# Kernel optimization log

Measured on AMD Instinct MI355X. Metric: run time of the kernel, lower is better.

## Reference

```python
import jax, jax.numpy as jnp
import numpy as np

B, S, H = 2, 2048, 4096
NH, NKV, HD = 32, 8, 128
ROPE_THETA = 10000.0


def _rope_tables(seq_len, head_dim, theta):
    inv_freq = 1.0 / (theta ** (jnp.arange(0, head_dim, 2, dtype=jnp.float32) / head_dim))
    t = jnp.arange(seq_len, dtype=jnp.float32)
    freqs = jnp.outer(t, inv_freq)            # [S, HD/2]
    emb = jnp.concatenate([freqs, freqs], axis=-1)  # [S, HD]
    return jnp.cos(emb), jnp.sin(emb)


def _rotate_half(x):
    x1, x2 = jnp.split(x, 2, axis=-1)
    return jnp.concatenate([-x2, x1], axis=-1)


def setup_inputs() -> dict:
    key = jax.random.key(0)
    ks = jax.random.split(key, 5)
    hidden_states = jax.random.normal(ks[0], (B, S, H), dtype=jnp.float32)
    # causal additive mask [B,1,S,S]
    neg = jnp.finfo(jnp.float32).min
    causal = jnp.where(jnp.tril(jnp.ones((S, S), dtype=bool)), 0.0, neg)
    attention_mask = jnp.broadcast_to(causal[None, None], (B, 1, S, S)).astype(jnp.float32)
    position_ids = jnp.broadcast_to(jnp.arange(S, dtype=jnp.int64)[None], (B, S))
    scale = 0.02
    Wq = jax.random.normal(ks[1], (H, H), dtype=jnp.float32) * scale
    Wk = jax.random.normal(ks[2], (NKV * HD, H), dtype=jnp.float32) * scale
    Wv = jax.random.normal(ks[3], (NKV * HD, H), dtype=jnp.float32) * scale
    Wo = jax.random.normal(ks[4], (H, H), dtype=jnp.float32) * scale
    return {"hidden_states": hidden_states, "attention_mask": attention_mask,
            "position_ids": position_ids, "Wq": Wq, "Wk": Wk, "Wv": Wv, "Wo": Wo}


def reference(hidden_states, attention_mask, position_ids, Wq, Wk, Wv, Wo):
    bsz, q_len, _ = hidden_states.shape
    # projections (nn.Linear: x @ W.T)
    q = (hidden_states @ Wq.T).reshape(bsz, q_len, NH, HD).transpose(0, 2, 1, 3)    # [B,NH,S,HD]
    k = (hidden_states @ Wk.T).reshape(bsz, q_len, NKV, HD).transpose(0, 2, 1, 3)   # [B,NKV,S,HD]
    v = (hidden_states @ Wv.T).reshape(bsz, q_len, NKV, HD).transpose(0, 2, 1, 3)
    # RoPE
    cos, sin = _rope_tables(q_len, HD, ROPE_THETA)
    cos = cos[position_ids][:, None]   # [B,1,S,HD]
    sin = sin[position_ids][:, None]
    q = q * cos + _rotate_half(q) * sin
    k = k * cos + _rotate_half(k) * sin
    # repeat_kv (GQA): [B,NKV,S,HD] -> [B,NH,S,HD]
    n_rep = NH // NKV
    k = jnp.repeat(k, n_rep, axis=1)
    v = jnp.repeat(v, n_rep, axis=1)
    # attention
    attn = jnp.einsum('bhqd,bhkd->bhqk', q, k) / jnp.sqrt(jnp.float32(HD))
    attn = attn + attention_mask
    attn = jax.nn.softmax(attn.astype(jnp.float32), axis=-1).astype(q.dtype)
    out = jnp.einsum('bhqk,bhkd->bhqd', attn, v)           # [B,NH,S,HD]
    out = out.transpose(0, 2, 1, 3).reshape(bsz, q_len, NH * HD)
    return out @ Wo.T
```

## Files before the change

kernel.cpp:

```cpp
#include <hip/hip_runtime.h>
#include <hip/hip_bf16.h>


typedef __bf16 bf16;
typedef __bf16 bf16x8 __attribute__((ext_vector_type(8)));
typedef float f32x4 __attribute__((ext_vector_type(4)));

#define UNROLL _Pragma("unroll")

__device__ __forceinline__ void async16(const bf16* g, bf16* l) {
  __builtin_amdgcn_global_load_lds(
      (const __attribute__((address_space(1))) void*)g,
      (__attribute__((address_space(3))) void*)l,
      16, 0, 0);
}

#define BARR { __builtin_amdgcn_s_barrier(); }
#define VMCNT(n) { asm volatile("s_waitcnt vmcnt(" #n ")" ::: "memory"); }

__global__ void k_cvt(const float* __restrict__ s, bf16* __restrict__ d, int n8) {
  int i = blockIdx.x * 256 + threadIdx.x;
  if (i >= n8) return;
  const float4* sp = (const float4*)s + (size_t)i * 2;
  float4 a = sp[0], b = sp[1];
  bf16x8 o = { (bf16)a.x, (bf16)a.y, (bf16)a.z, (bf16)a.w,
               (bf16)b.x, (bf16)b.y, (bf16)b.z, (bf16)b.w };
  *(bf16x8*)(d + (size_t)i * 8) = o;
}

__global__ void k_cvtw3(const float* __restrict__ Wq, const float* __restrict__ Wk,
                        const float* __restrict__ Wv, bf16* __restrict__ Wqkv) {
  int u = blockIdx.x * 256 + threadIdx.x;
  const float* sp;
  bf16* dp;
  size_t off;
  if (u < 2097152) { sp = Wq; dp = Wqkv; off = u; }
  else if (u < 2621440) { sp = Wk; dp = Wqkv + 16777216u; off = u - 2097152; }
  else { sp = Wv; dp = Wqkv + 20971520u; off = u - 2621440; }
  const float4* s4 = (const float4*)sp + off * 2;
  float4 a = s4[0], b = s4[1];
  bf16x8 o = { (bf16)a.x, (bf16)a.y, (bf16)a.z, (bf16)a.w,
               (bf16)b.x, (bf16)b.y, (bf16)b.z, (bf16)b.w };
  *(bf16x8*)(dp + off * 8) = o;
}

template <typename OutT, int SPLIT>
__global__ __launch_bounds__(512, 2) void k_gemmCS(
    const bf16* __restrict__ A, const bf16* __restrict__ Bw,
    OutT* __restrict__ C, int lda, int Kloop, int ldc, int nbx, size_t csplit) {
  __shared__ __align__(16) bf16 lds[2][4][8192];
  const int tid = threadIdx.x;
  const int lane = tid & 63;
  const int w = tid >> 6;
  const int wm = w >> 2, wn = w & 3;
  const int l16 = lane & 15, lh = lane >> 4;

  const int cpx = gridDim.x >> 3;
  const int swz = (blockIdx.x & 7) * cpx + (blockIdx.x >> 3);
  int by, bx;
  if (SPLIT) {
    const int kh = swz >> 7;
    const int t = swz & 127;
    by = t >> 3;
    bx = t & 7;
    A += (size_t)kh * 2048;
    Bw += (size_t)kh * 2048;
    C += (size_t)kh * csplit;
  } else {
    by = swz / nbx;
    bx = swz % nbx;
  }
  const size_t m0 = (size_t)by * 256, n0 = (size_t)bx * 256;

  const int row0 = tid >> 2;
  const int cOff = ((tid & 3) ^ ((row0 >> 1) & 3)) * 8;
  const bf16* pA0 = A + (m0 + row0) * lda + cOff;
  const bf16* pA1 = pA0 + (size_t)128 * lda;
  const bf16* pB0 = Bw + (n0 + row0) * lda + cOff;
  const bf16* pB1 = pB0 + (size_t)128 * lda;

#define SA(s, h, t)                                        \
  { const int kk = (t) * 64 + (h) * 32;                    \
    async16(pA0 + kk, &lds[s][h][0] + tid * 8);            \
    async16(pA1 + kk, &lds[s][h][0] + 4096 + tid * 8); }
#define SB(s, h, t)                                        \
  { const int kk = (t) * 64 + (h) * 32;                    \
    async16(pB0 + kk, &lds[s][2 + (h)][0] + tid * 8);      \
    async16(pB1 + kk, &lds[s][2 + (h)][0] + 4096 + tid * 8); }

#define RDA(s, u, mh)                                                 \
  UNROLL for (int x = 0; x < 4; ++x) {                                \
    int p = (wm * 128 + (mh) * 64 + x * 16 + l16) * 64 + lh * 16;     \
    p ^= ((p >> 7) & 3) << 4;                                         \
    Ar[x] = *(const bf16x8*)((const char*)&lds[s][u][0] + p);         \
  }
#define RDB(s, u)                                                     \
  UNROLL for (int y = 0; y < 4; ++y) {                                \
    int p = (wn * 64 + y * 16 + l16) * 64 + lh * 16;                  \
    p ^= ((p >> 7) & 3) << 4;                                         \
    Br[y] = *(const bf16x8*)((const char*)&lds[s][u][0] + p);         \
  }
#define MF(mh)                                                        \
  { __builtin_amdgcn_s_setprio(1);                                    \
    UNROLL for (int x = 0; x < 4; ++x)                                \
      UNROLL for (int y = 0; y < 4; ++y)                              \
        acc[(mh) * 4 + x][y] = __builtin_amdgcn_mfma_f32_16x16x32_bf16( \
            Ar[x], Br[y], acc[(mh) * 4 + x][y], 0, 0, 0);             \
    __builtin_amdgcn_s_setprio(0); }

  f32x4 acc[8][4] = {};
  const int NITER = Kloop >> 7;

  SA(0, 0, 0); SB(0, 0, 0); SA(0, 1, 0); SB(0, 1, 0); SA(1, 0, 1); SB(1, 0, 1);
  VMCNT(8);

#define ITER_BODY(i, LAST)                                                  \
  { const int t0 = 2 * (i), t1 = t0 + 1;                                    \
    bf16x8 Ar[4], Br[4];                                                    \
    BARR; RDA(0, 0, 0); RDB(0, 2); SA(1, 1, t1); MF(0);                     \
    BARR; RDA(0, 0, 1); SB(1, 1, t1); MF(1); VMCNT(8);                      \
    BARR; RDA(0, 1, 0); RDB(0, 3); if (!(LAST)) SA(0, 0, t0 + 2); MF(0);    \
    BARR; RDA(0, 1, 1); if (!(LAST)) SB(0, 0, t0 + 2); MF(1);               \
    if (LAST) { VMCNT(4); } else { VMCNT(8); }                              \
    BARR; RDA(1, 0, 0); RDB(1, 2); if (!(LAST)) SA(0, 1, t0 + 2); MF(0);    \
    BARR; RDA(1, 0, 1); if (!(LAST)) SB(0, 1, t0 + 2); MF(1);               \
    if (LAST) { VMCNT(0); } else { VMCNT(8); }                              \
    BARR; RDA(1, 1, 0); RDB(1, 3); if (!(LAST)) SA(1, 0, t1 + 2); MF(0);    \
    BARR; RDA(1, 1, 1); if (!(LAST)) SB(1, 0, t1 + 2); MF(1);               \
    if (!(LAST)) VMCNT(8); }

  for (int i = 0; i < NITER - 1; ++i) ITER_BODY(i, 0);
  ITER_BODY(NITER - 1, 1);

  UNROLL for (int mi = 0; mi < 8; ++mi) {
    size_t row = m0 + wm * 128 + mi * 16 + lh * 4;
    UNROLL for (int ni = 0; ni < 4; ++ni) {
      size_t col = n0 + wn * 64 + ni * 16 + l16;
      UNROLL for (int j = 0; j < 4; ++j)
        C[(row + j) * ldc + col] = (OutT)acc[mi][ni][j];
    }
  }
#undef SA
#undef SB
#undef RDA
#undef RDB
#undef MF
#undef ITER_BODY
}

__global__ void k_redsum(const bf16* __restrict__ s, bf16* __restrict__ QKV) {
  int i = blockIdx.x * 256 + threadIdx.x;
  int e = i * 8;
  int tok = e >> 11;
  int c = e & 2047;
  bf16x8 a = *(const bf16x8*)(s + e);
  bf16x8 b = *(const bf16x8*)(s + 8388608 + e);
  bf16x8 o;
  UNROLL for (int j = 0; j < 8; ++j) o[j] = (bf16)((float)a[j] + (float)b[j]);
  *(bf16x8*)(QKV + (size_t)tok * 6144 + 4096 + c) = o;
}

__global__ void k_rope(const bf16* __restrict__ QKV, bf16* __restrict__ Qr,
                       bf16* __restrict__ Kr) {
  int gid = blockIdx.x * 256 + threadIdx.x;
  int seg = gid & 7;
  int rest = gid >> 3;
  int slot = rest % 40;
  int tok = rest / 40;
  int s = tok & 2047;
  int b = tok >> 11;
  const bf16* src = QKV + (size_t)tok * 6144 + slot * 128 + seg * 8;
  bf16x8 a = *(const bf16x8*)src;
  bf16x8 c = *(const bf16x8*)(src + 64);
  bf16x8 o1v, o2v;
  const float scale = (slot < 32) ? 0.08838834764831845f : 1.0f;
  UNROLL for (int j = 0; j < 8; ++j) {
    int p = seg * 8 + j;
    float f = exp2f((float)p * (-13.287712379549449f / 64.0f));
    float sn, cn;
    sincosf((float)s * f, &sn, &cn);
    float x1 = (float)a[j], x2 = (float)c[j];
    o1v[j] = (bf16)((x1 * cn - x2 * sn) * scale);
    o2v[j] = (bf16)((x2 * cn + x1 * sn) * scale);
  }
  bf16* dst;
  if (slot < 32) {
    dst = Qr + (((size_t)b * 32 + slot) * 2048 + s) * 128 + seg * 8;
  } else {
    dst = Kr + (((size_t)b * 8 + (slot - 32)) * 2048 + s) * 128 + seg * 8;
  }
  *(bf16x8*)dst = o1v;
  *(bf16x8*)(dst + 64) = o2v;
}

__global__ void k_vtrans(const bf16* __restrict__ QKV, bf16* __restrict__ Vtg) {
  __shared__ __align__(16) bf16 T[64 * 64];
  const int tid = threadIdx.x;
  const int dt = blockIdx.x & 1;
  const int st = (blockIdx.x >> 1) & 31;
  const int hh = blockIdx.x >> 6;
  const int hkv = hh & 7, b = hh >> 3;
  const int s0 = st * 64, d0 = dt * 64;
  const bf16* src = QKV + (size_t)(b * 2048 + s0) * 6144 + 5120 + hkv * 128 + d0;
  UNROLL for (int k = 0; k < 2; ++k) {
    int cc = tid * 2 + k;
    int r = cc >> 3, c8 = cc & 7;
    bf16x8 v = *(const bf16x8*)(src + (size_t)r * 6144 + c8 * 8);
    int byte = (r * 128 + c8 * 16) ^ ((r & 7) << 4);
    *(bf16x8*)((char*)T + byte) = v;
  }
  __syncthreads();
  bf16* dst = Vtg + ((size_t)(b * 8 + hkv) * 128 + d0) * 2048 + s0;
  UNROLL for (int k = 0; k < 2; ++k) {
    int cc = tid * 2 + k;
    int d = cc >> 3, s8 = cc & 7;
    bf16x8 v;
    UNROLL for (int j = 0; j < 8; ++j) {
      int s = s8 * 8 + j;
      int byte = (s * 128 + d * 2) ^ ((s & 7) << 4);
      v[j] = *(const bf16*)((const char*)T + byte);
    }
    *(bf16x8*)(dst + (size_t)d * 2048 + s8 * 8) = v;
  }
}

__global__ __launch_bounds__(256, 2) void k_flash(
    const bf16* __restrict__ Qr, const bf16* __restrict__ Kr,
    const bf16* __restrict__ Vtg, bf16* __restrict__ Out) {
  __shared__ __align__(16) bf16 Kl[2][64 * 128];
  __shared__ __align__(16) bf16 Vl[2][128 * 64];
  __shared__ __align__(16) bf16 Pl[4][32 * 64];
  const int tid = threadIdx.x;
  const int lane = tid & 63;
  const int w = tid >> 6;
  const int l16 = lane & 15, lh = lane >> 4;
  const int bid = blockIdx.x;
  const int stream = ((bid >> 8) << 3) | (bid & 7);
  const int inner = (bid >> 3) & 31;
  const int b = stream >> 3;
  const int hkv = stream & 7;
  const int h = hkv * 4 + (inner >> 3);
  const int pid = inner & 7;
  const bf16* Kbase = Kr + ((size_t)stream) * 2048 * 128;
  const bf16* Vbase = Vtg + ((size_t)stream) * 128 * 2048;
  bf16* P = &Pl[w][0];

  int kOff[4], vOff[4], ldsOff[4];
  UNROLL for (int i = 0; i < 4; ++i) {
    int c = (w * 4 + i) * 64 + lane;
    ldsOff[i] = c * 8;
    int r = c >> 4, p = c & 15;
    kOff[i] = r * 128 + (p ^ (r & 7)) * 8;
    int r2 = c >> 3, p2 = c & 7;
    vOff[i] = r2 * 2048 + (p2 ^ (r2 & 7)) * 8;
  }

  for (int qi = 0; qi < 2; ++qi) {
    const int q = qi ? (15 - pid) : pid;
    const int q0 = q * 128;
    const int nt = 2 * q + 2;

    bf16x8 qf[2][4];
    UNROLL for (int m = 0; m < 2; ++m) {
      const bf16* qb = Qr + (((size_t)(b * 32 + h)) * 2048 + q0 + w * 32 + m * 16 + l16) * 128 + lh * 8;
      UNROLL for (int kc = 0; kc < 4; ++kc) qf[m][kc] = *(const bf16x8*)(qb + kc * 32);
    }
    f32x4 acc[2][8] = {};
    float mrow[2][4] = {{-1e30f, -1e30f, -1e30f, -1e30f}, {-1e30f, -1e30f, -1e30f, -1e30f}};
    float lrow[2][4] = {};

    UNROLL for (int i = 0; i < 4; ++i) {
      async16(Kbase + kOff[i], &Kl[0][0] + ldsOff[i]);
      async16(Vbase + vOff[i], &Vl[0][0] + ldsOff[i]);
    }
    __syncthreads();

    for (int t = 0; t < nt; ++t) {
      const int cur = t & 1;
      if (t + 1 < nt) {
        const int nb = t + 1;
        UNROLL for (int i = 0; i < 4; ++i) {
          async16(Kbase + (size_t)nb * 8192 + kOff[i], &Kl[cur ^ 1][0] + ldsOff[i]);
          async16(Vbase + (size_t)nb * 64 + vOff[i], &Vl[cur ^ 1][0] + ldsOff[i]);
        }
      }
      f32x4 sf[2][4] = {};
      UNROLL for (int ni = 0; ni < 4; ++ni) {
        int row = ni * 16 + l16;
        bf16x8 kf[4];
        UNROLL for (int kc = 0; kc < 4; ++kc) {
          int byte = (row * 256 + kc * 64 + lh * 16) ^ ((row & 7) << 4);
          kf[kc] = *(const bf16x8*)((const char*)&Kl[cur][0] + byte);
        }
        UNROLL for (int m = 0; m < 2; ++m)
          UNROLL for (int kc = 0; kc < 4; ++kc)
            sf[m][ni] = __builtin_amdgcn_mfma_f32_16x16x32_bf16(qf[m][kc], kf[kc], sf[m][ni], 0, 0, 0);
      }
      if (t >= 2 * q) {
        UNROLL for (int m = 0; m < 2; ++m)
          UNROLL for (int ni = 0; ni < 4; ++ni) {
            int key = t * 64 + ni * 16 + l16;
            UNROLL for (int j = 0; j < 4; ++j) {
              int rowg = q0 + w * 32 + m * 16 + lh * 4 + j;
              if (key > rowg) sf[m][ni][j] = -1e30f;
            }
          }
      }
      float corr[2][4];
      UNROLL for (int m = 0; m < 2; ++m)
        UNROLL for (int j = 0; j < 4; ++j) {
          float mx = fmaxf(fmaxf(sf[m][0][j], sf[m][1][j]), fmaxf(sf[m][2][j], sf[m][3][j]));
          mx = fmaxf(mx, __shfl_xor(mx, 1));
          mx = fmaxf(mx, __shfl_xor(mx, 2));
          mx = fmaxf(mx, __shfl_xor(mx, 4));
          mx = fmaxf(mx, __shfl_xor(mx, 8));
          float mn = fmaxf(mrow[m][j], mx);
          corr[m][j] = __expf(mrow[m][j] - mn);
          mrow[m][j] = mn;
          float rs = 0.f;
          UNROLL for (int ni = 0; ni < 4; ++ni) {
            float pv = __expf(sf[m][ni][j] - mn);
            sf[m][ni][j] = pv;
            rs += pv;
          }
          rs += __shfl_xor(rs, 1);
          rs += __shfl_xor(rs, 2);
          rs += __shfl_xor(rs, 4);
          rs += __shfl_xor(rs, 8);
          lrow[m][j] = lrow[m][j] * corr[m][j] + rs;
        }
      UNROLL for (int m = 0; m < 2; ++m)
        UNROLL for (int di = 0; di < 8; ++di)
          UNROLL for (int j = 0; j < 4; ++j) acc[m][di][j] *= corr[m][j];
      UNROLL for (int m = 0; m < 2; ++m)
        UNROLL for (int ni = 0; ni < 4; ++ni)
          UNROLL for (int j = 0; j < 4; ++j) {
            int row = m * 16 + lh * 4 + j;
            int byte = (row * 128 + ni * 32 + l16 * 2) ^ ((row & 7) << 4);
            *(bf16*)((char*)P + byte) = (bf16)sf[m][ni][j];
          }
      UNROLL for (int kc = 0; kc < 2; ++kc) {
        bf16x8 pa[2];
        UNROLL for (int m = 0; m < 2; ++m) {
          int row = m * 16 + l16;
          int byte = (row * 128 + kc * 64 + lh * 16) ^ ((row & 7) << 4);
          pa[m] = *(const bf16x8*)((const char*)P + byte);
        }
        UNROLL for (int di = 0; di < 8; ++di) {
          int d = di * 16 + l16;
          int byte = (d * 128 + kc * 64 + lh * 16) ^ ((d & 7) << 4);
          bf16x8 vb = *(const bf16x8*)((const char*)&Vl[cur][0] + byte);
          UNROLL for (int m = 0; m < 2; ++m)
            acc[m][di] = __builtin_amdgcn_mfma_f32_16x16x32_bf16(pa[m], vb, acc[m][di], 0, 0, 0);
        }
      }
      __syncthreads();
    }

    UNROLL for (int m = 0; m < 2; ++m)
      UNROLL for (int j = 0; j < 4; ++j) {
        float inv = 1.0f / lrow[m][j];
        int rowg = q0 + w * 32 + m * 16 + lh * 4 + j;
        bf16* ob = Out + ((size_t)(b * 2048) + rowg) * 4096 + h * 128 + l16;
        UNROLL for (int di = 0; di < 8; ++di)
          ob[di * 16] = (bf16)(acc[m][di][j] * inv);
      }
  }
}

extern "C" void kernel_launch(void* const* d_in, const int* in_sizes, int n_in,
                              void* d_out, int out_size, void* d_ws, size_t ws_size,
                              hipStream_t stream) {
  const float* hidden = (const float*)d_in[0];
  const float* Wq = (const float*)d_in[3];
  const float* Wk = (const float*)d_in[4];
  const float* Wv = (const float*)d_in[5];
  const float* Wo = (const float*)d_in[6];
  float* out = (float*)d_out;

  char* ws = (char*)d_ws;
  if (ws_size < 184549376u) return;
  bf16* Xb = (bf16*)(ws);
  bf16* Wqkv = (bf16*)(ws + 33554432u);
  bf16* QKV = (bf16*)(ws + 83886080u);
  bf16* Qr = (bf16*)(ws + 134217728u);
  bf16* Kr = (bf16*)(ws + 167772160u);
  bf16* Vtg = (bf16*)(ws + 176160768u);
  bf16* AttnO = Xb;
  bf16* Wob = Wqkv;
  bf16* Spart = Qr;

  k_cvt<<<8192, 256, 0, stream>>>(hidden, Xb, 2097152);
  k_cvtw3<<<12288, 256, 0, stream>>>(Wq, Wk, Wv, Wqkv);
  k_gemmCS<bf16, 0><<<256, 512, 0, stream>>>(Xb, Wqkv, QKV, 4096, 4096, 6144, 16, 0);
  k_gemmCS<bf16, 1><<<256, 512, 0, stream>>>(
      Xb, Wqkv + (size_t)4096 * 4096, Spart, 4096, 2048, 2048, 8, 8388608u);
  k_redsum<<<4096, 256, 0, stream>>>(Spart, QKV);
  k_rope<<<5120, 256, 0, stream>>>(QKV, Qr, Kr);
  k_vtrans<<<1024, 256, 0, stream>>>(QKV, Vtg);
  k_cvt<<<8192, 256, 0, stream>>>(Wo, Wob, 2097152);
  k_flash<<<512, 256, 0, stream>>>(Qr, Kr, Vtg, AttnO);
  k_gemmCS<float, 0><<<256, 512, 0, stream>>>(AttnO, Wob, out, 4096, 4096, 4096, 16, 0);
}
```

Before: 555.2 us.

## Software-pipeline attention loop: overlap next QK^T MFMA with current softmax/PV

Restructures the flash-attention inner loop so the QK^T MFMAs for tile t run alongside the softmax and PV work for tile t-1, using two ping-pong score register sets and a two-stage K/V prefetch schedule with explicit vmcnt waits and barriers. It also folds log2(e) into the Q scale during RoPE so the softmax can use exp2f in place of __expf. The aim is to hide softmax latency behind matrix-core work and reduce exp cost, at the price of more live registers, which may lower occupancy. The loop is unrolled by two with a prologue and epilogue, which makes the buffer indexing and the number of LDS buffers in use more delicate.

```diff
diff --git a/kernel.cpp b/kernel.cpp
--- a/kernel.cpp
+++ b/kernel.cpp
@@ -173,7 +173,7 @@
   bf16x8 a = *(const bf16x8*)src;
   bf16x8 c = *(const bf16x8*)(src + 64);
   bf16x8 o1v, o2v;
-  const float scale = (slot < 32) ? 0.08838834764831845f : 1.0f;
+  const float scale = (slot < 32) ? 0.12751743f : 1.0f;
   UNROLL for (int j = 0; j < 8; ++j) {
     int p = seg * 8 + j;
     float f = exp2f((float)p * (-13.287712379549449f / 64.0f));
@@ -255,6 +255,99 @@
     vOff[i] = r2 * 2048 + (p2 ^ (r2 & 7)) * 8;
   }
 
+#define STAGEK(buf, nb)                                                      \
+  UNROLL for (int i = 0; i < 4; ++i)                                         \
+    async16(Kbase + (size_t)(nb) * 8192 + kOff[i], &Kl[buf][0] + ldsOff[i]);
+#define STAGEV(buf, nb)                                                      \
+  UNROLL for (int i = 0; i < 4; ++i)                                         \
+    async16(Vbase + (size_t)(nb) * 64 + vOff[i], &Vl[buf][0] + ldsOff[i]);
+
+#define QKM(tt, SF)                                                          \
+  { const int cc = (tt) & 1;                                                 \
+    UNROLL for (int ni = 0; ni < 4; ++ni) {                                  \
+      int row = ni * 16 + l16;                                               \
+      bf16x8 kf[4];                                                          \
+      UNROLL for (int kc = 0; kc < 4; ++kc) {                                \
+        int byte = (row * 256 + kc * 64 + lh * 16) ^ ((row & 7) << 4);       \
+        kf[kc] = *(const bf16x8*)((const char*)&Kl[cc][0] + byte);           \
+      }                                                                      \
+      UNROLL for (int m = 0; m < 2; ++m) {                                   \
+        f32x4 t0 = {0.f, 0.f, 0.f, 0.f};                                     \
+        UNROLL for (int kc = 0; kc < 4; ++kc)                                \
+          t0 = __builtin_amdgcn_mfma_f32_16x16x32_bf16(qf[m][kc], kf[kc], t0, 0, 0, 0); \
+        SF[m][ni] = t0;                                                      \
+      }                                                                      \
+    } }
+
+#define SMPV(tt, SF)                                                         \
+  { const int cc = (tt) & 1;                                                 \
+    if ((tt) >= 2 * q) {                                                     \
+      UNROLL for (int m = 0; m < 2; ++m)                                     \
+        UNROLL for (int ni = 0; ni < 4; ++ni) {                              \
+          int key = (tt) * 64 + ni * 16 + l16;                               \
+          UNROLL for (int j = 0; j < 4; ++j) {                               \
+            int rowg = q0 + w * 32 + m * 16 + lh * 4 + j;                    \
+            if (key > rowg) SF[m][ni][j] = -1e30f;                           \
+          }                                                                  \
+        }                                                                    \
+    }                                                                        \
+    float corr[2][4];                                                        \
+    UNROLL for (int m = 0; m < 2; ++m)                                       \
+      UNROLL for (int j = 0; j < 4; ++j) {                                   \
+        float mx = fmaxf(fmaxf(SF[m][0][j], SF[m][1][j]),                    \
+                         fmaxf(SF[m][2][j], SF[m][3][j]));                   \
+        mx = fmaxf(mx, __shfl_xor(mx, 1));                                   \
+        mx = fmaxf(mx, __shfl_xor(mx, 2));                                   \
+        mx = fmaxf(mx, __shfl_xor(mx, 4));                                   \
+        mx = fmaxf(mx, __shfl_xor(mx, 8));                                   \
+        float mn = fmaxf(mrow[m][j], mx);                                    \
+        corr[m][j] = exp2f(mrow[m][j] - mn);                                 \
+        mrow[m][j] = mn;                                                     \
+        float rs = 0.f;                                                      \
+        UNROLL for (int ni = 0; ni < 4; ++ni) {                              \
+          float pv = exp2f(SF[m][ni][j] - mn);                               \
+          SF[m][ni][j] = pv;                                                 \
+          rs += pv;                                                          \
+        }                                                                    \
+        rs += __shfl_xor(rs, 1);                                             \
+        rs += __shfl_xor(rs, 2);                                             \
+        rs += __shfl_xor(rs, 4);                                             \
+        rs += __shfl_xor(rs, 8);                                             \
+        lrow[m][j] = lrow[m][j] * corr[m][j] + rs;                           \
+      }                                                                      \
+    UNROLL for (int m = 0; m < 2; ++m)                                       \
+      UNROLL for (int di = 0; di < 8; ++di)                                  \
+        UNROLL for (int j = 0; j < 4; ++j) acc[m][di][j] *= corr[m][j];      \
+    UNROLL for (int m = 0; m < 2; ++m)                                       \
+      UNROLL for (int ni = 0; ni < 4; ++ni)                                  \
+        UNROLL for (int j = 0; j < 4; ++j) {                                 \
+          int row = m * 16 + lh * 4 + j;                                     \
+          int byte = (row * 128 + ni * 32 + l16 * 2) ^ ((row & 7) << 4);     \
+          *(bf16*)((char*)P + byte) = (bf16)SF[m][ni][j];                    \
+        }                                                                    \
+    UNROLL for (int kc = 0; kc < 2; ++kc) {                                  \
+      bf16x8 pa[2];                                                          \
+      UNROLL for (int m = 0; m < 2; ++m) {                                   \
+        int row = m * 16 + l16;                                              \
+        int byte = (row * 128 + kc * 64 + lh * 16) ^ ((row & 7) << 4);       \
+        pa[m] = *(const bf16x8*)((const char*)P + byte);                     \
+      }                                                                      \
+      UNROLL for (int di = 0; di < 8; ++di) {                                \
+        int d = di * 16 + l16;                                               \
+        int byte = (d * 128 + kc * 64 + lh * 16) ^ ((d & 7) << 4);           \
+        bf16x8 vb = *(const bf16x8*)((const char*)&Vl[cc][0] + byte);        \
+        UNROLL for (int m = 0; m < 2; ++m)                                   \
+          acc[m][di] = __builtin_amdgcn_mfma_f32_16x16x32_bf16(pa[m], vb, acc[m][di], 0, 0, 0); \
+      }                                                                      \
+    } }
+
+#define BODY(tt, SFC, SFP)                                                   \
+  { if ((tt) + 1 < nt) STAGEK(((tt) + 1) & 1, (tt) + 1);                     \
+    STAGEV((tt) & 1, (tt));                                                  \
+    QKM((tt), SFC);                                                          \
+    SMPV((tt) - 1, SFP);                                                     \
+    VMCNT(0); BARR; }
+
   for (int qi = 0; qi < 2; ++qi) {
     const int q = qi ? (15 - pid) : pid;
     const int q0 = q * 128;
@@ -266,96 +359,26 @@
       UNROLL for (int kc = 0; kc < 4; ++kc) qf[m][kc] = *(const bf16x8*)(qb + kc * 32);
     }
     f32x4 acc[2][8] = {};
+    f32x4 sfA[2][4], sfB[2][4];
     float mrow[2][4] = {{-1e30f, -1e30f, -1e30f, -1e30f}, {-1e30f, -1e30f, -1e30f, -1e30f}};
     float lrow[2][4] = {};
 
-    UNROLL for (int i = 0; i < 4; ++i) {
-      async16(Kbase + kOff[i], &Kl[0][0] + ldsOff[i]);
-      async16(Vbase + vOff[i], &Vl[0][0] + ldsOff[i]);
+    STAGEK(0, 0);
+    if (nt > 1) STAGEK(1, 1);
+    STAGEV(0, 0);
+    VMCNT(0);
+    BARR;
+    QKM(0, sfA);
+    BARR;
+
+    int t = 1;
+    for (; t + 1 < nt; t += 2) {
+      BODY(t, sfB, sfA);
+      BODY(t + 1, sfA, sfB);
     }
-    __syncthreads();
-
-    for (int t = 0; t < nt; ++t) {
-      const int cur = t & 1;
-      if (t + 1 < nt) {
-        const int nb = t + 1;
-        UNROLL for (int i = 0; i < 4; ++i) {
-          async16(Kbase + (size_t)nb * 8192 + kOff[i], &Kl[cur ^ 1][0] + ldsOff[i]);
-          async16(Vbase + (size_t)nb * 64 + vOff[i], &Vl[cur ^ 1][0] + ldsOff[i]);
-        }
-      }
-      f32x4 sf[2][4] = {};
-      UNROLL for (int ni = 0; ni < 4; ++ni) {
-        int row = ni * 16 + l16;
-        bf16x8 kf[4];
-        UNROLL for (int kc = 0; kc < 4; ++kc) {
-          int byte = (row * 256 + kc * 64 + lh * 16) ^ ((row & 7) << 4);
-          kf[kc] = *(const bf16x8*)((const char*)&Kl[cur][0] + byte);
-        }
-        UNROLL for (int m = 0; m < 2; ++m)
-          UNROLL for (int kc = 0; kc < 4; ++kc)
-            sf[m][ni] = __builtin_amdgcn_mfma_f32_16x16x32_bf16(qf[m][kc], kf[kc], sf[m][ni], 0, 0, 0);
-      }
-      if (t >= 2 * q) {
-        UNROLL for (int m = 0; m < 2; ++m)
-          UNROLL for (int ni = 0; ni < 4; ++ni) {
-            int key = t * 64 + ni * 16 + l16;
-            UNROLL for (int j = 0; j < 4; ++j) {
-              int rowg = q0 + w * 32 + m * 16 + lh * 4 + j;
-              if (key > rowg) sf[m][ni][j] = -1e30f;
-            }
-          }
-      }
-      float corr[2][4];
-      UNROLL for (int m = 0; m < 2; ++m)
-        UNROLL for (int j = 0; j < 4; ++j) {
-          float mx = fmaxf(fmaxf(sf[m][0][j], sf[m][1][j]), fmaxf(sf[m][2][j], sf[m][3][j]));
-          mx = fmaxf(mx, __shfl_xor(mx, 1));
-          mx = fmaxf(mx, __shfl_xor(mx, 2));
-          mx = fmaxf(mx, __shfl_xor(mx, 4));
-          mx = fmaxf(mx, __shfl_xor(mx, 8));
-          float mn = fmaxf(mrow[m][j], mx);
-          corr[m][j] = __expf(mrow[m][j] - mn);
-          mrow[m][j] = mn;
-          float rs = 0.f;
-          UNROLL for (int ni = 0; ni < 4; ++ni) {
-            float pv = __expf(sf[m][ni][j] - mn);
-            sf[m][ni][j] = pv;
-            rs += pv;
-          }
-          rs += __shfl_xor(rs, 1);
-          rs += __shfl_xor(rs, 2);
-          rs += __shfl_xor(rs, 4);
-          rs += __shfl_xor(rs, 8);
-          lrow[m][j] = lrow[m][j] * corr[m][j] + rs;
-        }
-      UNROLL for (int m = 0; m < 2; ++m)
-        UNROLL for (int di = 0; di < 8; ++di)
-          UNROLL for (int j = 0; j < 4; ++j) acc[m][di][j] *= corr[m][j];
-      UNROLL for (int m = 0; m < 2; ++m)
-        UNROLL for (int ni = 0; ni < 4; ++ni)
-          UNROLL for (int j = 0; j < 4; ++j) {
-            int row = m * 16 + lh * 4 + j;
-            int byte = (row * 128 + ni * 32 + l16 * 2) ^ ((row & 7) << 4);
-            *(bf16*)((char*)P + byte) = (bf16)sf[m][ni][j];
-          }
-      UNROLL for (int kc = 0; kc < 2; ++kc) {
-        bf16x8 pa[2];
-        UNROLL for (int m = 0; m < 2; ++m) {
-          int row = m * 16 + l16;
-          int byte = (row * 128 + kc * 64 + lh * 16) ^ ((row & 7) << 4);
-          pa[m] = *(const bf16x8*)((const char*)P + byte);
-        }
-        UNROLL for (int di = 0; di < 8; ++di) {
-          int d = di * 16 + l16;
-          int byte = (d * 128 + kc * 64 + lh * 16) ^ ((d & 7) << 4);
-          bf16x8 vb = *(const bf16x8*)((const char*)&Vl[cur][0] + byte);
-          UNROLL for (int m = 0; m < 2; ++m)
-            acc[m][di] = __builtin_amdgcn_mfma_f32_16x16x32_bf16(pa[m], vb, acc[m][di], 0, 0, 0);
-        }
-      }
-      __syncthreads();
-    }
+    BODY(nt - 1, sfB, sfA);
+    SMPV(nt - 1, sfB);
+    BARR;
 
     UNROLL for (int m = 0; m < 2; ++m)
       UNROLL for (int j = 0; j < 4; ++j) {
@@ -366,6 +389,11 @@
           ob[di * 16] = (bf16)(acc[m][di][j] * inv);
       }
   }
+#undef STAGEK
+#undef STAGEV
+#undef QKM
+#undef SMPV
+#undef BODY
 }
 
 extern "C" void kernel_launch(void* const* d_in, const int* in_sizes, int n_in,
```

After: 1.014 ms. +82.7%, slower.
